# Optimization experiments

Hardware: AMD Instinct MI355X
Metric: run time of the kernel (lower is better)

## Reference

```python
import jax, jax.numpy as jnp
import numpy as np

N_NODES = 50000
N_EDGES = 800000


def setup_inputs() -> dict:
    key = jax.random.key(0)
    ks = jax.random.split(key, 6)
    x = jax.random.normal(ks[0], (N_NODES, 22), dtype=jnp.float32)
    # small weight scale to keep tanh in its linear-ish regime
    W0 = jax.random.normal(ks[1], (22, 220), dtype=jnp.float32) * 0.1
    W1 = jax.random.normal(ks[2], (220, 220), dtype=jnp.float32) * 0.05
    W2 = jax.random.normal(ks[3], (220, 220), dtype=jnp.float32) * 0.05
    W3 = jax.random.normal(ks[4], (220, 10), dtype=jnp.float32) * 0.05
    b0 = jnp.zeros((220,), jnp.float32)
    b1 = jnp.zeros((220,), jnp.float32)
    b2 = jnp.zeros((220,), jnp.float32)
    b3 = jnp.zeros((10,), jnp.float32)
    edge_index = jax.random.randint(ks[5], (2, N_EDGES), 0, N_NODES, dtype=jnp.int64)
    return {"x": x, "W0": W0, "b0": b0, "W1": W1, "b1": b1,
            "W2": W2, "b2": b2, "W3": W3, "b3": b3, "edge_index": edge_index}


def _graph_conv(h, W, b, src, dst, inv_sqrt_out, inv_sqrt_in, activation):
    # DGL GraphConv, norm='both':
    #   h' = D_in^{-1/2} * A^T * (D_out^{-1/2} * h) @ W + b
    h = h * inv_sqrt_out[:, None]          # [N, F_in]
    m = h[src]                             # gather: [E, F_in]
    agg = jax.ops.segment_sum(m, dst, num_segments=N_NODES)  # scatter-add: [N, F_in]
    agg = agg * inv_sqrt_in[:, None]
    out = agg @ W + b
    if activation is not None:
        out = activation(out)
    return out


def reference(x, W0, b0, W1, b1, W2, b2, W3, b3, edge_index):
    src, dst = edge_index[0], edge_index[1]
    ones = jnp.ones((edge_index.shape[1],), jnp.float32)
    deg_out = jax.ops.segment_sum(ones, src, num_segments=N_NODES)
    deg_in = jax.ops.segment_sum(ones, dst, num_segments=N_NODES)
    inv_sqrt_out = jax.lax.rsqrt(jnp.maximum(deg_out, 1.0))
    inv_sqrt_in = jax.lax.rsqrt(jnp.maximum(deg_in, 1.0))

    h = _graph_conv(x, W0, b0, src, dst, inv_sqrt_out, inv_sqrt_in, jnp.tanh)
    h = _graph_conv(h, W1, b1, src, dst, inv_sqrt_out, inv_sqrt_in, jnp.tanh)
    h = _graph_conv(h, W2, b2, src, dst, inv_sqrt_out, inv_sqrt_in, jnp.tanh)
    h = _graph_conv(h, W3, b3, src, dst, inv_sqrt_out, inv_sqrt_in, None)
    return h
```

## Files before the change

### kernel.cpp

```cpp
#include <hip/hip_runtime.h>
#include <math.h>

#define N_NODES 50000
#define N_EDGES 800000
#define NPAD 50176
#define HSTR 224

typedef __attribute__((ext_vector_type(8))) short short8;
typedef __attribute__((ext_vector_type(4))) float f32x4;
typedef __attribute__((ext_vector_type(4))) _Float16 half4;


__device__ __forceinline__ float fast_tanh(float x) {
    float e = __expf(2.0f * x);
    float r = __builtin_amdgcn_rcpf(e + 1.0f);
    return 1.0f - 2.0f * r;
}

__device__ __forceinline__ unsigned short rne_bf16(float x) {
    unsigned u = __builtin_bit_cast(unsigned, x);
    return (unsigned short)((u + 0x7FFFu + ((u >> 16) & 1u)) >> 16);
}

__device__ __forceinline__ void split_bf16(float x, unsigned short& hi, unsigned short& lo) {
    hi = rne_bf16(x);
    float hf = __builtin_bit_cast(float, (unsigned)hi << 16);
    lo = rne_bf16(x - hf);
}

__device__ __forceinline__ f32x4 mfma16(short8 a, short8 b, f32x4 c) {
    return __builtin_amdgcn_mfma_f32_16x16x32_bf16(a, b, c, 0, 0, 0);
}

__device__ __forceinline__ void wsplit_one(const float* __restrict__ W, int KIN, int LDA,
                                           unsigned short* __restrict__ WT_hi,
                                           unsigned short* __restrict__ WT_lo, int idx) {
    int n = idx / LDA;
    int k = idx - n * LDA;
    float v = (n < 220 && k < KIN) ? W[k * 220 + n] : 0.f;
    unsigned short hi, lo;
    split_bf16(v, hi, lo);
    WT_hi[idx] = hi;
    WT_lo[idx] = lo;
}


__global__ void k_hist_wsplit(const int* __restrict__ ei, int* __restrict__ deg8,
                              int* __restrict__ cnt8, int* __restrict__ rank,
                              const float* __restrict__ W0, const float* __restrict__ W1,
                              const float* __restrict__ W2,
                              unsigned short* __restrict__ wt0h, unsigned short* __restrict__ wt0l,
                              unsigned short* __restrict__ wt1h, unsigned short* __restrict__ wt1l,
                              unsigned short* __restrict__ wt2h, unsigned short* __restrict__ wt2l) {
    int bx = blockIdx.x;
    if (bx < 782) {
        int c = bx & 7;
        int* degc = deg8 + c * NPAD;
        int* cntc = cnt8 + c * NPAD;
        int base = bx * 1024 + threadIdx.x;
#pragma unroll
        for (int i = 0; i < 4; ++i) {
            int e = base + i * 256;
            if (e < N_EDGES) {
                atomicAdd(&degc[ei[e]], 1);
                int r = atomicAdd(&cntc[ei[N_EDGES + e]], 1);
                rank[e] = (r << 3) | c;
            }
        }
    } else if (bx < 810) {
        int idx = (bx - 782) * 256 + threadIdx.x;
        if (idx < 224 * 32) wsplit_one(W0, 22, 32, wt0h, wt0l, idx);
    } else if (bx < 1006) {
        int idx = (bx - 810) * 256 + threadIdx.x;
        wsplit_one(W1, 220, 224, wt1h, wt1l, idx);
    } else {
        int idx = (bx - 1006) * 256 + threadIdx.x;
        wsplit_one(W2, 220, 224, wt2h, wt2l, idx);
    }
}

__global__ void k_sum8(int* __restrict__ cnt8, const int* __restrict__ deg8,
                       int* __restrict__ ecsbuf, int* __restrict__ deg_out) {
    int d = blockIdx.x * 256 + threadIdx.x;
    if (d >= NPAD) return;
    int s = 0;
#pragma unroll
    for (int c = 0; c < 8; ++c) {
        int v = cnt8[c * NPAD + d];
        cnt8[c * NPAD + d] = s;
        s += v;
    }
    ecsbuf[1 + d] = s;
    if (d == 0) ecsbuf[0] = 0;
    int t = 0;
#pragma unroll
    for (int c = 0; c < 8; ++c) t += deg8[c * NPAD + d];
    deg_out[d] = t;
}

__global__ void k_scan1(const int* __restrict__ in, int* __restrict__ out,
                        int* __restrict__ bsum, int n) {
    __shared__ int s[256];
    int i = blockIdx.x * 256 + threadIdx.x;
    int v = (i < n) ? in[i] : 0;
    s[threadIdx.x] = v;
    __syncthreads();
    for (int off = 1; off < 256; off <<= 1) {
        int t = (threadIdx.x >= off) ? s[threadIdx.x - off] : 0;
        __syncthreads();
        s[threadIdx.x] += t;
        __syncthreads();
    }
    if (i < n) out[i] = s[threadIdx.x] - v;
    if (threadIdx.x == 255 && bsum) bsum[blockIdx.x] = s[255];
}

__global__ void k_scan_mid(int* __restrict__ a, int n) {
    __shared__ int s[256];
    __shared__ int carry;
    if (threadIdx.x == 0) carry = 0;
    for (int base = 0; base < n; base += 256) {
        int i = base + threadIdx.x;
        int v = (i < n) ? a[i] : 0;
        s[threadIdx.x] = v;
        __syncthreads();
        for (int off = 1; off < 256; off <<= 1) {
            int t = (threadIdx.x >= off) ? s[threadIdx.x - off] : 0;
            __syncthreads();
            s[threadIdx.x] += t;
            __syncthreads();
        }
        int c = carry;
        if (i < n) a[i] = s[threadIdx.x] - v + c;
        __syncthreads();
        if (threadIdx.x == 0) carry = c + s[255];
        __syncthreads();
    }
}

__global__ void k_scan3(int* __restrict__ out, const int* __restrict__ bscan, int n) {
    int i = blockIdx.x * 256 + threadIdx.x;
    if (i < n) out[i] += bscan[blockIdx.x];
}

__global__ void k_post_scan(const int* __restrict__ ei, const int* __restrict__ ecsbuf,
                            const int* __restrict__ rank, const int* __restrict__ prefix8,
                            const int* __restrict__ deg_out, const float* __restrict__ x,
                            float* __restrict__ inv_out, float* __restrict__ inv_in,
                            int* __restrict__ src_sorted, float* __restrict__ xs) {
    int bx = blockIdx.x;
    if (bx < 196) {
        int n = bx * 256 + threadIdx.x;
        if (n >= N_NODES) return;
        int di = ecsbuf[n + 2] - ecsbuf[n + 1];
        int a = deg_out[n]; if (a < 1) a = 1;
        if (di < 1) di = 1;
        inv_out[n] = 1.0f / sqrtf((float)a);
        inv_in[n]  = 1.0f / sqrtf((float)di);
    } else if (bx < 3321) {
        int e = (bx - 196) * 256 + threadIdx.x;
        if (e < N_EDGES) {
            int d = ei[N_EDGES + e];
            int rc = rank[e];
            int c = rc & 7, r = rc >> 3;
            src_sorted[ecsbuf[1 + d] + prefix8[c * NPAD + d] + r] = ei[e];
        }
    } else {
        int idx = (bx - 3321) * 256 + threadIdx.x;
        if (idx >= N_NODES * 11) return;
        int n = idx / 11;
        int f2 = idx - n * 11;
        int a = deg_out[n]; if (a < 1) a = 1;
        float sc = 1.0f / sqrtf((float)a);
        float2 v = *(const float2*)&x[n * 22 + f2 * 2];
        v.x *= sc; v.y *= sc;
        *(float2*)&xs[n * 22 + f2 * 2] = v;
    }
}


__global__ void k_agg22_split(const float* __restrict__ xs,
                              const int* __restrict__ ecsbuf, const int* __restrict__ srcs,
                              const float* __restrict__ inv_in,
                              unsigned short* __restrict__ A_hi, unsigned short* __restrict__ A_lo) {
    int idx = blockIdx.x * 256 + threadIdx.x;
    int n = idx >> 4, f2 = idx & 15;
    if (n >= N_NODES) return;
    float ax = 0.f, ay = 0.f;
    if (f2 <= 10) {
        const float2* xb = (const float2*)(xs) + f2;
        int e = ecsbuf[n + 1], end = ecsbuf[n + 2];
        for (; e + 3 < end; e += 4) {
            int s0 = srcs[e], s1 = srcs[e + 1], s2 = srcs[e + 2], s3 = srcs[e + 3];
            float2 v0 = xb[s0 * 11], v1 = xb[s1 * 11];
            float2 v2 = xb[s2 * 11], v3 = xb[s3 * 11];
            ax += (v0.x + v1.x) + (v2.x + v3.x);
            ay += (v0.y + v1.y) + (v2.y + v3.y);
        }
        for (; e < end; ++e) {
            float2 v0 = xb[srcs[e] * 11];
            ax += v0.x;
            ay += v0.y;
        }
        float si = inv_in[n];
        ax *= si; ay *= si;
    }
    ushort2 h2, l2;
    split_bf16(ax, h2.x, l2.x);
    split_bf16(ay, h2.y, l2.y);
    *(ushort2*)&A_hi[n * 32 + f2 * 2] = h2;
    *(ushort2*)&A_lo[n * 32 + f2 * 2] = l2;
}

__global__ __launch_bounds__(256) void k_agg220_split(const _Float16* __restrict__ h,
                                                      const int* __restrict__ ecsbuf,
                                                      const int* __restrict__ srcs,
                                                      const float* __restrict__ inv_in,
                                                      unsigned short* __restrict__ A_hi,
                                                      unsigned short* __restrict__ A_lo) {
    int lane = threadIdx.x & 63;
    int n = blockIdx.x * 4 + (threadIdx.x >> 6);
    if (n >= N_NODES || lane >= 56) return;
    size_t ob = (size_t)n * 224 + lane * 4;
    if (lane == 55) {
        ushort4 z = {0, 0, 0, 0};
        *(ushort4*)&A_hi[ob] = z;
        *(ushort4*)&A_lo[ob] = z;
        return;
    }
    int f4 = lane * 4;
    const _Float16* hb = h + f4;
    int e = ecsbuf[n + 1], end = ecsbuf[n + 2];
    float4 a0 = {0,0,0,0}, a1 = {0,0,0,0}, a2 = {0,0,0,0}, a3 = {0,0,0,0};
    for (; e + 7 < end; e += 8) {
        int s0 = srcs[e],     s1 = srcs[e + 1], s2 = srcs[e + 2], s3 = srcs[e + 3];
        int s4 = srcs[e + 4], s5 = srcs[e + 5], s6 = srcs[e + 6], s7 = srcs[e + 7];
        half4 v0 = *(const half4*)(hb + (size_t)s0 * HSTR);
        half4 v1 = *(const half4*)(hb + (size_t)s1 * HSTR);
        half4 v2 = *(const half4*)(hb + (size_t)s2 * HSTR);
        half4 v3 = *(const half4*)(hb + (size_t)s3 * HSTR);
        half4 v4 = *(const half4*)(hb + (size_t)s4 * HSTR);
        half4 v5 = *(const half4*)(hb + (size_t)s5 * HSTR);
        half4 v6 = *(const half4*)(hb + (size_t)s6 * HSTR);
        half4 v7 = *(const half4*)(hb + (size_t)s7 * HSTR);
        a0.x += (float)v0.x; a0.y += (float)v0.y; a0.z += (float)v0.z; a0.w += (float)v0.w;
        a1.x += (float)v1.x; a1.y += (float)v1.y; a1.z += (float)v1.z; a1.w += (float)v1.w;
        a2.x += (float)v2.x; a2.y += (float)v2.y; a2.z += (float)v2.z; a2.w += (float)v2.w;
        a3.x += (float)v3.x; a3.y += (float)v3.y; a3.z += (float)v3.z; a3.w += (float)v3.w;
        a0.x += (float)v4.x; a0.y += (float)v4.y; a0.z += (float)v4.z; a0.w += (float)v4.w;
        a1.x += (float)v5.x; a1.y += (float)v5.y; a1.z += (float)v5.z; a1.w += (float)v5.w;
        a2.x += (float)v6.x; a2.y += (float)v6.y; a2.z += (float)v6.z; a2.w += (float)v6.w;
        a3.x += (float)v7.x; a3.y += (float)v7.y; a3.z += (float)v7.z; a3.w += (float)v7.w;
    }
    for (; e + 3 < end; e += 4) {
        int s0 = srcs[e], s1 = srcs[e + 1], s2 = srcs[e + 2], s3 = srcs[e + 3];
        half4 v0 = *(const half4*)(hb + (size_t)s0 * HSTR);
        half4 v1 = *(const half4*)(hb + (size_t)s1 * HSTR);
        half4 v2 = *(const half4*)(hb + (size_t)s2 * HSTR);
        half4 v3 = *(const half4*)(hb + (size_t)s3 * HSTR);
        a0.x += (float)v0.x; a0.y += (float)v0.y; a0.z += (float)v0.z; a0.w += (float)v0.w;
        a1.x += (float)v1.x; a1.y += (float)v1.y; a1.z += (float)v1.z; a1.w += (float)v1.w;
        a2.x += (float)v2.x; a2.y += (float)v2.y; a2.z += (float)v2.z; a2.w += (float)v2.w;
        a3.x += (float)v3.x; a3.y += (float)v3.y; a3.z += (float)v3.z; a3.w += (float)v3.w;
    }
    for (; e < end; ++e) {
        half4 v = *(const half4*)(hb + (size_t)srcs[e] * HSTR);
        a0.x += (float)v.x; a0.y += (float)v.y; a0.z += (float)v.z; a0.w += (float)v.w;
    }
    float sc = inv_in[n];
    float4 t;
    t.x = ((a0.x + a1.x) + (a2.x + a3.x)) * sc;
    t.y = ((a0.y + a1.y) + (a2.y + a3.y)) * sc;
    t.z = ((a0.z + a1.z) + (a2.z + a3.z)) * sc;
    t.w = ((a0.w + a1.w) + (a2.w + a3.w)) * sc;
    ushort4 h4, l4;
    split_bf16(t.x, h4.x, l4.x);
    split_bf16(t.y, h4.y, l4.y);
    split_bf16(t.z, h4.z, l4.z);
    split_bf16(t.w, h4.w, l4.w);
    *(ushort4*)&A_hi[ob] = h4;
    *(ushort4*)&A_lo[ob] = l4;
}

__global__ void k_agg10_epi(const float* __restrict__ tmp, const int* __restrict__ ecsbuf,
                            const int* __restrict__ srcs, const float* __restrict__ inv_in,
                            const float* __restrict__ bias, float* __restrict__ out) {
    int idx = blockIdx.x * 256 + threadIdx.x;
    if (idx >= N_NODES * 5) return;
    int n = idx / 5;
    int f2 = idx - n * 5;
    const float2* tb0 = (const float2*)(tmp) + f2;
    const float2* tb1 = (const float2*)(tmp + (size_t)NPAD * 10) + f2;
    float ax = 0.f, ay = 0.f;
    int e = ecsbuf[n + 1], end = ecsbuf[n + 2];
    for (; e + 1 < end; e += 2) {
        float2 u0 = tb0[srcs[e] * 5],     w0 = tb1[srcs[e] * 5];
        float2 u1 = tb0[srcs[e + 1] * 5], w1 = tb1[srcs[e + 1] * 5];
        ax += (u0.x + w0.x) + (u1.x + w1.x);
        ay += (u0.y + w0.y) + (u1.y + w1.y);
    }
    if (e < end) {
        float2 u0 = tb0[srcs[e] * 5], w0 = tb1[srcs[e] * 5];
        ax += u0.x + w0.x;
        ay += u0.y + w0.y;
    }
    float si = inv_in[n];
    float2 o;
    o.x = ax * si + bias[f2 * 2];
    o.y = ay * si + bias[f2 * 2 + 1];
    *(float2*)&out[n * 10 + f2 * 2] = o;
}

template <int KSTEPS, int LDA, bool FUSE_W3>
__global__ __launch_bounds__(256, 4) void k_gemm_mfma(const unsigned short* __restrict__ A_hi,
                                                      const unsigned short* __restrict__ A_lo,
                                                      const unsigned short* __restrict__ WT_hi,
                                                      const unsigned short* __restrict__ WT_lo,
                                                      const float* __restrict__ bias,
                                                      const float* __restrict__ post,
                                                      _Float16* __restrict__ out,
                                                      const float* __restrict__ W3,
                                                      float* __restrict__ tmp) {
    int tid = threadIdx.x;
    int l = tid & 63, w = tid >> 6;
    int lrow = l & 15, q = l >> 4;
    int bid = blockIdx.x;
    int ch = bid & 1;
    int rt = (bid >> 1) * 64 + w * 16;
    int cb = ch * 112;

    const unsigned short* pah = A_hi + (size_t)(rt + lrow) * LDA + q * 8;
    const unsigned short* pal = A_lo + (size_t)(rt + lrow) * LDA + q * 8;
    const unsigned short* pbh = WT_hi + (size_t)(cb + lrow) * LDA + q * 8;
    const unsigned short* pbl = WT_lo + (size_t)(cb + lrow) * LDA + q * 8;

    f32x4 acc[7];
#pragma unroll
    for (int ct = 0; ct < 7; ++ct) acc[ct] = (f32x4){0.f, 0.f, 0.f, 0.f};

#pragma unroll
    for (int ks = 0; ks < KSTEPS; ++ks) {
        int k0 = ks * 32;
        short8 ah = *(const short8*)(const void*)(pah + k0);
        short8 al = *(const short8*)(const void*)(pal + k0);
#pragma unroll
        for (int ct = 0; ct < 7; ++ct) {
            size_t boff = (size_t)(ct * 16) * LDA + k0;
            short8 bh = *(const short8*)(const void*)(pbh + boff);
            short8 bl = *(const short8*)(const void*)(pbl + boff);
            acc[ct] = mfma16(ah, bh, acc[ct]);
            acc[ct] = mfma16(ah, bl, acc[ct]);
            acc[ct] = mfma16(al, bh, acc[ct]);
        }
    }

    float pv[4];
#pragma unroll
    for (int r = 0; r < 4; ++r) {
        int r0 = rt + q * 4 + r;
        pv[r] = (r0 < N_NODES) ? post[r0] : 0.f;
    }

    if (!FUSE_W3) {
#pragma unroll
        for (int ct = 0; ct < 7; ++ct) {
            int col = cb + ct * 16 + lrow;
            if (col >= 220) continue;
            float bv = bias[col];
#pragma unroll
            for (int r = 0; r < 4; ++r) {
                int r0 = rt + q * 4 + r;
                if (r0 < N_NODES)
                    out[(size_t)r0 * HSTR + col] = (_Float16)(pv[r] * fast_tanh(acc[ct][r] + bv));
            }
        }
    } else {
        float p[4][10];
#pragma unroll
        for (int r = 0; r < 4; ++r)
#pragma unroll
            for (int j = 0; j < 10; ++j) p[r][j] = 0.f;
#pragma unroll
        for (int ct = 0; ct < 7; ++ct) {
            int col = cb + ct * 16 + lrow;
            bool cok = col < 220;
            float bv = cok ? bias[col] : 0.f;
            float w3v[10];
            if (cok) {
                const float2* wp = (const float2*)&W3[col * 10];
#pragma unroll
                for (int j2 = 0; j2 < 5; ++j2) {
                    float2 t = wp[j2];
                    w3v[2 * j2] = t.x;
                    w3v[2 * j2 + 1] = t.y;
                }
            } else {
#pragma unroll
                for (int j = 0; j < 10; ++j) w3v[j] = 0.f;
            }
#pragma unroll
            for (int r = 0; r < 4; ++r) {
                float h2 = pv[r] * fast_tanh(acc[ct][r] + bv);
#pragma unroll
                for (int j = 0; j < 10; ++j) p[r][j] += h2 * w3v[j];
            }
        }
#pragma unroll
        for (int r = 0; r < 4; ++r)
#pragma unroll
            for (int j = 0; j < 10; ++j) {
                float v = p[r][j];
                v += __shfl_xor(v, 1, 64);
                v += __shfl_xor(v, 2, 64);
                v += __shfl_xor(v, 4, 64);
                v += __shfl_xor(v, 8, 64);
                p[r][j] = v;
            }
        if (lrow == 0) {
#pragma unroll
            for (int r = 0; r < 4; ++r) {
                int row = rt + q * 4 + r;
                if (row < N_NODES) {
                    float* tp = tmp + ((size_t)ch * NPAD + row) * 10;
#pragma unroll
                    for (int j2 = 0; j2 < 5; ++j2) {
                        float2 o = {p[r][2 * j2], p[r][2 * j2 + 1]};
                        *(float2*)&tp[2 * j2] = o;
                    }
                }
            }
        }
    }
}


extern "C" void kernel_launch(void* const* d_in, const int* in_sizes, int n_in,
                              void* d_out, int out_size, void* d_ws, size_t ws_size,
                              hipStream_t stream) {
    const float* x  = (const float*)d_in[0];
    const float* W0 = (const float*)d_in[1];
    const float* b0 = (const float*)d_in[2];
    const float* W1 = (const float*)d_in[3];
    const float* b1 = (const float*)d_in[4];
    const float* W2 = (const float*)d_in[5];
    const float* b2 = (const float*)d_in[6];
    const float* W3 = (const float*)d_in[7];
    const float* b3 = (const float*)d_in[8];
    const int*   ei = (const int*)d_in[9];
    float* out = (float*)d_out;

    int* ws = (int*)d_ws;
    int* ecsbuf     = ws + 0;
    int* deg_out    = ws + 50432;
    int* bsumA      = ws + 100608;
    float* inv_out  = (float*)(ws + 100864);
    float* inv_in   = (float*)(ws + 151040);
    int* src_sorted = ws + 201216;
    unsigned short* wt0h = (unsigned short*)(ws + 1001216);
    unsigned short* wt0l = (unsigned short*)(ws + 1004800);
    unsigned short* wt1h = (unsigned short*)(ws + 1008384);
    unsigned short* wt1l = (unsigned short*)(ws + 1033472);
    unsigned short* wt2h = (unsigned short*)(ws + 1058560);
    unsigned short* wt2l = (unsigned short*)(ws + 1083648);
    unsigned short* ahi  = (unsigned short*)(ws + 1108736);
    unsigned short* alo  = (unsigned short*)(ws + 6728448);
    _Float16* hbuf = (_Float16*)(ws + 12348160);
    float* tmp10 = (float*)(ws + 17948160);
    int* rank  = (int*)ahi;
    int* cnt8  = (int*)alo;
    int* deg8  = (int*)alo + 8 * NPAD;
    float* xs  = (float*)(ws + 1108736 + 3000000);

    hipMemsetAsync(cnt8, 0, (size_t)16 * NPAD * sizeof(int), stream);

    k_hist_wsplit<<<1202, 256, 0, stream>>>(ei, deg8, cnt8, rank,
                                            W0, W1, W2, wt0h, wt0l, wt1h, wt1l, wt2h, wt2l);
    k_sum8<<<196, 256, 0, stream>>>(cnt8, deg8, ecsbuf, deg_out);
    k_scan1<<<196, 256, 0, stream>>>(ecsbuf + 1, ecsbuf + 1, bsumA, NPAD);
    k_scan_mid<<<1, 256, 0, stream>>>(bsumA, 196);
    k_scan3<<<196, 256, 0, stream>>>(ecsbuf + 1, bsumA, NPAD);
    k_post_scan<<<5470, 256, 0, stream>>>(ei, ecsbuf, rank, cnt8, deg_out, x,
                                          inv_out, inv_in, src_sorted, xs);

    int gemm_grid = (NPAD / 64) * 2;
    int agg_grid  = (N_NODES + 3) / 4;

    k_agg22_split<<<(N_NODES * 16 + 255) / 256, 256, 0, stream>>>(
        xs, ecsbuf, src_sorted, inv_in, ahi, alo);
    k_gemm_mfma<1, 32, false><<<gemm_grid, 256, 0, stream>>>(
        ahi, alo, wt0h, wt0l, b0, inv_out, hbuf, nullptr, nullptr);

    k_agg220_split<<<agg_grid, 256, 0, stream>>>(hbuf, ecsbuf, src_sorted, inv_in, ahi, alo);
    k_gemm_mfma<7, 224, false><<<gemm_grid, 256, 0, stream>>>(
        ahi, alo, wt1h, wt1l, b1, inv_out, hbuf, nullptr, nullptr);

    k_agg220_split<<<agg_grid, 256, 0, stream>>>(hbuf, ecsbuf, src_sorted, inv_in, ahi, alo);
    k_gemm_mfma<7, 224, true><<<gemm_grid, 256, 0, stream>>>(
        ahi, alo, wt2h, wt2l, b2, inv_out, nullptr, W3, tmp10);

    k_agg10_epi<<<(N_NODES * 5 + 255) / 256, 256, 0, stream>>>(
        tmp10, ecsbuf, src_sorted, inv_in, b3, out);
}
```

Before: 466.2 us.

## Use LDS-privatized out-degree histogram and swizzle GEMM row-tile mapping

The out-degree count no longer uses global atomics per edge. Instead, 196 blocks each build a 1024-node shared-memory histogram over a quarter of the edges and write the partial counts, and k_sum8 adds the four partials. This drops the 8-way replicated global deg array and shrinks the memset. Separately, the 220-wide GEMMs remap block and wave indices to an interleaved row pattern, which changes which A rows each block and wave handle, likely for cache or channel locality. The cost is that each histogram block reads 200k edges, about 50x redundant reads of the src array overall.

```diff
diff --git a/kernel.cpp b/kernel.cpp
--- a/kernel.cpp
+++ b/kernel.cpp
@@ -45,41 +45,54 @@
 }
 
 
-__global__ void k_hist_wsplit(const int* __restrict__ ei, int* __restrict__ deg8,
-                              int* __restrict__ cnt8, int* __restrict__ rank,
-                              const float* __restrict__ W0, const float* __restrict__ W1,
-                              const float* __restrict__ W2,
-                              unsigned short* __restrict__ wt0h, unsigned short* __restrict__ wt0l,
-                              unsigned short* __restrict__ wt1h, unsigned short* __restrict__ wt1l,
-                              unsigned short* __restrict__ wt2h, unsigned short* __restrict__ wt2l) {
+__global__ void k_build(const int* __restrict__ ei, int* __restrict__ deg_part,
+                        int* __restrict__ cnt8, int* __restrict__ rank,
+                        const float* __restrict__ W0, const float* __restrict__ W1,
+                        const float* __restrict__ W2,
+                        unsigned short* __restrict__ wt0h, unsigned short* __restrict__ wt0l,
+                        unsigned short* __restrict__ wt1h, unsigned short* __restrict__ wt1l,
+                        unsigned short* __restrict__ wt2h, unsigned short* __restrict__ wt2l) {
     int bx = blockIdx.x;
     if (bx < 782) {
         int c = bx & 7;
-        int* degc = deg8 + c * NPAD;
         int* cntc = cnt8 + c * NPAD;
         int base = bx * 1024 + threadIdx.x;
 #pragma unroll
         for (int i = 0; i < 4; ++i) {
             int e = base + i * 256;
             if (e < N_EDGES) {
-                atomicAdd(&degc[ei[e]], 1);
                 int r = atomicAdd(&cntc[ei[N_EDGES + e]], 1);
                 rank[e] = (r << 3) | c;
             }
         }
-    } else if (bx < 810) {
-        int idx = (bx - 782) * 256 + threadIdx.x;
+    } else if (bx < 978) {
+        __shared__ int hcnt[1024];
+        int b2 = bx - 782;
+        int rng = b2 >> 2, chk = b2 & 3;
+        int lo = rng << 10;
+        for (int i = threadIdx.x; i < 1024; i += 256) hcnt[i] = 0;
+        __syncthreads();
+        int ebeg = chk * 200000, eend = ebeg + 200000;
+        for (int e = ebeg + threadIdx.x; e < eend; e += 256) {
+            int sdx = ei[e] - lo;
+            if ((unsigned)sdx < 1024u) atomicAdd(&hcnt[sdx], 1);
+        }
+        __syncthreads();
+        for (int i = threadIdx.x; i < 1024; i += 256)
+            deg_part[chk * NPAD + lo + i] = hcnt[i];
+    } else if (bx < 1006) {
+        int idx = (bx - 978) * 256 + threadIdx.x;
         if (idx < 224 * 32) wsplit_one(W0, 22, 32, wt0h, wt0l, idx);
-    } else if (bx < 1006) {
-        int idx = (bx - 810) * 256 + threadIdx.x;
+    } else if (bx < 1202) {
+        int idx = (bx - 1006) * 256 + threadIdx.x;
         wsplit_one(W1, 220, 224, wt1h, wt1l, idx);
     } else {
-        int idx = (bx - 1006) * 256 + threadIdx.x;
+        int idx = (bx - 1202) * 256 + threadIdx.x;
         wsplit_one(W2, 220, 224, wt2h, wt2l, idx);
     }
 }
 
-__global__ void k_sum8(int* __restrict__ cnt8, const int* __restrict__ deg8,
+__global__ void k_sum8(int* __restrict__ cnt8, const int* __restrict__ deg_part,
                        int* __restrict__ ecsbuf, int* __restrict__ deg_out) {
     int d = blockIdx.x * 256 + threadIdx.x;
     if (d >= NPAD) return;
@@ -92,10 +105,7 @@
     }
     ecsbuf[1 + d] = s;
     if (d == 0) ecsbuf[0] = 0;
-    int t = 0;
-#pragma unroll
-    for (int c = 0; c < 8; ++c) t += deg8[c * NPAD + d];
-    deg_out[d] = t;
+    deg_out[d] = deg_part[d] + deg_part[NPAD + d] + deg_part[2 * NPAD + d] + deg_part[3 * NPAD + d];
 }
 
 __global__ void k_scan1(const int* __restrict__ in, int* __restrict__ out,
@@ -321,16 +331,32 @@
                                                       _Float16* __restrict__ out,
                                                       const float* __restrict__ W3,
                                                       float* __restrict__ tmp) {
+    constexpr bool SWZ = (LDA == 224);
     int tid = threadIdx.x;
     int l = tid & 63, w = tid >> 6;
     int lrow = l & 15, q = l >> 4;
     int bid = blockIdx.x;
-    int ch = bid & 1;
-    int rt = (bid >> 1) * 64 + w * 16;
+
+    int ch, s = 0, v = 0, rt = 0;
+    if constexpr (SWZ) {
+        s = bid & 7;
+        int u = bid >> 3;
+        ch = u & 1;
+        v = u >> 1;
+    } else {
+        ch = bid & 1;
+        rt = (bid >> 1) * 64 + w * 16;
+    }
     int cb = ch * 112;
 
-    const unsigned short* pah = A_hi + (size_t)(rt + lrow) * LDA + q * 8;
-    const unsigned short* pal = A_lo + (size_t)(rt + lrow) * LDA + q * 8;
+    auto prow = [&](int i) -> int {
+        if constexpr (SWZ) return 4 * s + 512 * v + 32 * (4 * w + (i >> 2)) + (i & 3);
+        else return rt + i;
+    };
+
+    int arow = prow(lrow);
+    const unsigned short* pah = A_hi + (size_t)arow * LDA + q * 8;
+    const unsigned short* pal = A_lo + (size_t)arow * LDA + q * 8;
     const unsigned short* pbh = WT_hi + (size_t)(cb + lrow) * LDA + q * 8;
     const unsigned short* pbl = WT_lo + (size_t)(cb + lrow) * LDA + q * 8;
 
@@ -357,7 +383,7 @@
     float pv[4];
 #pragma unroll
     for (int r = 0; r < 4; ++r) {
-        int r0 = rt + q * 4 + r;
+        int r0 = prow(q * 4 + r);
         pv[r] = (r0 < N_NODES) ? post[r0] : 0.f;
     }
 
@@ -369,7 +395,7 @@
             float bv = bias[col];
 #pragma unroll
             for (int r = 0; r < 4; ++r) {
-                int r0 = rt + q * 4 + r;
+                int r0 = prow(q * 4 + r);
                 if (r0 < N_NODES)
                     out[(size_t)r0 * HSTR + col] = (_Float16)(pv[r] * fast_tanh(acc[ct][r] + bv));
             }
@@ -409,17 +435,17 @@
         for (int r = 0; r < 4; ++r)
 #pragma unroll
             for (int j = 0; j < 10; ++j) {
-                float v = p[r][j];
-                v += __shfl_xor(v, 1, 64);
-                v += __shfl_xor(v, 2, 64);
-                v += __shfl_xor(v, 4, 64);
-                v += __shfl_xor(v, 8, 64);
-                p[r][j] = v;
+                float vv = p[r][j];
+                vv += __shfl_xor(vv, 1, 64);
+                vv += __shfl_xor(vv, 2, 64);
+                vv += __shfl_xor(vv, 4, 64);
+                vv += __shfl_xor(vv, 8, 64);
+                p[r][j] = vv;
             }
         if (lrow == 0) {
 #pragma unroll
             for (int r = 0; r < 4; ++r) {
-                int row = rt + q * 4 + r;
+                int row = prow(q * 4 + r);
                 if (row < N_NODES) {
                     float* tp = tmp + ((size_t)ch * NPAD + row) * 10;
 #pragma unroll
@@ -466,16 +492,16 @@
     unsigned short* alo  = (unsigned short*)(ws + 6728448);
     _Float16* hbuf = (_Float16*)(ws + 12348160);
     float* tmp10 = (float*)(ws + 17948160);
-    int* rank  = (int*)ahi;
-    int* cnt8  = (int*)alo;
-    int* deg8  = (int*)alo + 8 * NPAD;
-    float* xs  = (float*)(ws + 1108736 + 3000000);
-
-    hipMemsetAsync(cnt8, 0, (size_t)16 * NPAD * sizeof(int), stream);
-
-    k_hist_wsplit<<<1202, 256, 0, stream>>>(ei, deg8, cnt8, rank,
-                                            W0, W1, W2, wt0h, wt0l, wt1h, wt1l, wt2h, wt2l);
-    k_sum8<<<196, 256, 0, stream>>>(cnt8, deg8, ecsbuf, deg_out);
+    int* rank     = (int*)ahi;
+    int* cnt8     = (int*)alo;
+    int* deg_part = (int*)alo + 8 * NPAD;
+    float* xs = (float*)(ws + 1108736 + 3000000);
+
+    hipMemsetAsync(cnt8, 0, (size_t)8 * NPAD * sizeof(int), stream);
+
+    k_build<<<1398, 256, 0, stream>>>(ei, deg_part, cnt8, rank,
+                                      W0, W1, W2, wt0h, wt0l, wt1h, wt1l, wt2h, wt2l);
+    k_sum8<<<196, 256, 0, stream>>>(cnt8, deg_part, ecsbuf, deg_out);
     k_scan1<<<196, 256, 0, stream>>>(ecsbuf + 1, ecsbuf + 1, bsumA, NPAD);
     k_scan_mid<<<1, 256, 0, stream>>>(bsumA, 196);
     k_scan3<<<196, 256, 0, stream>>>(ecsbuf + 1, bsumA, NPAD);
```

Measured after the change: 631.2 us. 1.35x slower.
